# Kernel tuning notes

Measured on AMD Instinct MI355X. Metric: run time of the kernel, lower is better.

## Reference

```python
import jax, jax.numpy as jnp
import numpy as np

T, B, D, H = 2048, 64, 512, 512

def setup_inputs() -> dict:
    key = jax.random.key(0)
    ks = jax.random.split(key, 5)
    scale = 1.0 / np.sqrt(D + H)  # ~ torch Linear init scale
    inputs = jax.random.normal(ks[0], (T, B, D), dtype=jnp.float32)
    Wf = jax.random.normal(ks[1], (D + H, H), dtype=jnp.float32) * scale
    Wi = jax.random.normal(ks[2], (D + H, H), dtype=jnp.float32) * scale
    Wg = jax.random.normal(ks[3], (D + H, H), dtype=jnp.float32) * scale
    Wo = jax.random.normal(ks[4], (D + H, H), dtype=jnp.float32) * scale
    z = jnp.zeros((H,), dtype=jnp.float32)
    return {"inputs": inputs, "Wf": Wf, "bf": z, "Wi": Wi, "bi": z,
            "Wg": Wg, "bg": z, "Wo": Wo, "bo": z}

def reference(inputs, Wf, bf, Wi, bi, Wg, bg, Wo, bo):
    # Fuse the 4 gate GEMMs into one [D+H, 4H] matmul per step (same math).
    W = jnp.concatenate([Wf, Wi, Wg, Wo], axis=1)          # [D+H, 4H]
    b = jnp.concatenate([bf, bi, bg, bo], axis=0)          # [4H]
    Hdim = Wf.shape[1]
    Bsz = inputs.shape[1]
    h0 = jnp.zeros((Bsz, Hdim), dtype=inputs.dtype)
    c0 = jnp.zeros((Bsz, Hdim), dtype=inputs.dtype)

    def step(carry, x):
        hx, cx = carry
        combined = jnp.concatenate([x, hx], axis=1)        # [B, D+H]
        gates = combined @ W + b                           # [B, 4H]
        f, i, g, o = jnp.split(gates, 4, axis=1)
        f = jax.nn.sigmoid(f)
        i = jax.nn.sigmoid(i)
        g = jnp.tanh(g)
        o = jax.nn.sigmoid(o)
        cx = f * cx + i * g
        hx = o * jnp.tanh(cx)
        return (hx, cx), hx

    (hT, cT), stacked = jax.lax.scan(step, (h0, c0), inputs)
    return stacked, (hT, cT)
```

## Files before the change

### kernel.cpp

```cpp
#include <hip/hip_runtime.h>
#include <hip/hip_bf16.h>


#define T_N 2048
#define B_N 64
#define D_N 512
#define H_N 512
#define DH_N 1024
#define NBLK 64
#define NHEAT 192
#define CPB 8
#define GCPB 32
#define NTHR 256

#define STACK_ELEMS ((size_t)T_N * B_N * H_N)
#define HT_OFF STACK_ELEMS
#define CT_OFF (STACK_ELEMS + (size_t)B_N * H_N)

typedef __attribute__((ext_vector_type(4))) float f32x4;
typedef __attribute__((ext_vector_type(8))) short bf16x8;

__device__ __forceinline__ unsigned short f2bf(float f) {
  union { __hip_bfloat16 h; unsigned short u; } u;
  u.h = __float2bfloat16(f);
  return u.u;
}
__device__ __forceinline__ float bf2f(unsigned short us) {
  union { unsigned u32; float f; } x;
  x.u32 = ((unsigned)us) << 16;
  return x.f;
}

__device__ __forceinline__ float sigf(float x) { return 1.0f / (1.0f + __expf(-x)); }
__device__ __forceinline__ float tanhfast(float x) { return 1.0f - 2.0f / (__expf(2.0f * x) + 1.0f); }

__global__ void init_ws_kernel(unsigned* ws32) {
  int i = blockIdx.x * blockDim.x + threadIdx.x;
  if (i < 65536) ws32[i] = 0u;
}

__global__ void xconv_kernel(const float* __restrict__ X, unsigned short* __restrict__ Xb) {
  size_t i = ((size_t)blockIdx.x * blockDim.x + threadIdx.x) * 8;
  float4 v0 = *(const float4*)(X + i);
  float4 v1 = *(const float4*)(X + i + 4);
  bf16x8 o;
  o[0] = (short)f2bf(v0.x); o[1] = (short)f2bf(v0.y);
  o[2] = (short)f2bf(v0.z); o[3] = (short)f2bf(v0.w);
  o[4] = (short)f2bf(v1.x); o[5] = (short)f2bf(v1.y);
  o[6] = (short)f2bf(v1.z); o[7] = (short)f2bf(v1.w);
  *(bf16x8*)(Xb + i) = o;
}

__device__ __forceinline__ void load_x_tile(const unsigned short* Xb, const float* X,
                                            int t, int arow, int kg, bf16x8 (&xa)[16]) {
  if (Xb) {
    const unsigned short* xp = Xb + ((size_t)t * B_N + arow) * D_N + kg;
#pragma unroll
    for (int kk = 0; kk < 16; ++kk) xa[kk] = *(const bf16x8*)(xp + kk * 32);
  } else {
    const float* xp = X + ((size_t)t * B_N + arow) * D_N + kg;
#pragma unroll
    for (int kk = 0; kk < 16; ++kk) {
      float4 v0 = *(const float4*)(xp + kk * 32);
      float4 v1 = *(const float4*)(xp + kk * 32 + 4);
      bf16x8 a;
      a[0] = (short)f2bf(v0.x); a[1] = (short)f2bf(v0.y);
      a[2] = (short)f2bf(v0.z); a[3] = (short)f2bf(v0.w);
      a[4] = (short)f2bf(v1.x); a[5] = (short)f2bf(v1.y);
      a[6] = (short)f2bf(v1.z); a[7] = (short)f2bf(v1.w);
      xa[kk] = a;
    }
  }
}

__global__ __launch_bounds__(NTHR, 1) void lstm_kernel(
    const float* __restrict__ X, const unsigned short* __restrict__ Xb,
    const float* __restrict__ Wf, const float* __restrict__ bF,
    const float* __restrict__ Wi, const float* __restrict__ bI,
    const float* __restrict__ Wg, const float* __restrict__ bG,
    const float* __restrict__ Wo, const float* __restrict__ bO,
    unsigned short* __restrict__ ring, unsigned* __restrict__ flags,
    float* __restrict__ out) {
  __shared__ unsigned short Wl[GCPB * DH_N];

  const int tid = threadIdx.x;
  const int blk = blockIdx.x;
  const int lane = tid & 63;

  if (blk >= NBLK) {
    const unsigned long long* fp = (const unsigned long long*)flags + (size_t)lane * 2;
    float a = 1.0f + (float)tid * 1e-7f;
    const float m = 0.99993f, c = 1e-8f;
    for (long i = 0;; ++i) {
#pragma unroll
      for (int j = 0; j < 512; ++j) a = __builtin_fmaf(a, m, c);
      if ((i & 63) == 0) {
        unsigned long long q0 = __hip_atomic_load(fp, __ATOMIC_RELAXED, __HIP_MEMORY_SCOPE_AGENT);
        unsigned long long q1 = __hip_atomic_load(fp + 1, __ATOMIC_RELAXED, __HIP_MEMORY_SCOPE_AGENT);
        unsigned a0 = (unsigned)q0, a1 = (unsigned)(q0 >> 32);
        unsigned a2 = (unsigned)q1, a3 = (unsigned)(q1 >> 32);
        bool ok = (a0 >= (unsigned)T_N) && (a1 >= (unsigned)T_N) &&
                  (a2 >= (unsigned)T_N) && (a3 >= (unsigned)T_N);
        if (__all((int)ok)) break;
        if (i > (1l << 21)) break;
      }
    }
    asm volatile("" :: "v"(a));
    return;
  }

  const int c0 = blk * CPB;
  const int w = tid >> 6;
  const int l16 = lane & 15;
  const int g16 = lane >> 4;

  for (int idx = tid; idx < GCPB * DH_N; idx += NTHR) {
    int k = idx >> 5;
    int cl = idx & 31;
    const float* wsrc = (cl < 8) ? Wf : (cl < 16) ? Wi : (cl < 24) ? Wg : Wo;
    float v = wsrc[(size_t)k * H_N + c0 + (cl & 7)];
    int pos = ((k >> 5) * 1024) + ((cl >> 4) * 512) + (((k >> 3) & 3) * 128) + ((cl & 15) * 8) + (k & 7);
    Wl[pos] = f2bf(v);
  }

  const int cc = l16 & 7;
  const float bias0 = (l16 < 8) ? bF[c0 + cc] : bI[c0 + cc];
  const float bias1 = (l16 < 8) ? bG[c0 + cc] : bO[c0 + cc];
  __syncthreads();

  const int arow = 16 * w + l16;
  const int kg = 8 * g16;
  const int lofs8 = lane * 8;
  const bool owner = (arow == blk);

  bf16x8 wb0[32], wb1[32];
#pragma unroll
  for (int K = 0; K < 32; ++K) {
    wb0[K] = *(const bf16x8*)&Wl[K * 1024 + lofs8];
    wb1[K] = *(const bf16x8*)&Wl[K * 1024 + 512 + lofs8];
  }

  float cst[4] = {0.f, 0.f, 0.f, 0.f};
  float hT_local[4] = {0.f, 0.f, 0.f, 0.f};

  bf16x8 xa[16];
  load_x_tile(Xb, X, 0, arow, kg, xa);

  for (int t = 0; t < T_N; ++t) {
    const int slotR = (t + 1) & 1;
    const int slotW = t & 1;

    f32x4 x0a = {0.f,0.f,0.f,0.f}, x0b = {0.f,0.f,0.f,0.f};
    f32x4 x1a = {0.f,0.f,0.f,0.f}, x1b = {0.f,0.f,0.f,0.f};
#pragma unroll
    for (int kk = 0; kk < 8; ++kk) {
      x0a = __builtin_amdgcn_mfma_f32_16x16x32_bf16(xa[kk], wb0[kk], x0a, 0, 0, 0);
      x1a = __builtin_amdgcn_mfma_f32_16x16x32_bf16(xa[kk], wb1[kk], x1a, 0, 0, 0);
    }
#pragma unroll
    for (int kk = 8; kk < 16; ++kk) {
      x0b = __builtin_amdgcn_mfma_f32_16x16x32_bf16(xa[kk], wb0[kk], x0b, 0, 0, 0);
      x1b = __builtin_amdgcn_mfma_f32_16x16x32_bf16(xa[kk], wb1[kk], x1b, 0, 0, 0);
    }

    if (t > 0) {
      const unsigned tgt = (unsigned)t;
      const unsigned long long* fp = (const unsigned long long*)flags + (size_t)lane * 2;
      long guard = 0;
      for (;;) {
        unsigned long long q0 = __hip_atomic_load(fp, __ATOMIC_RELAXED, __HIP_MEMORY_SCOPE_AGENT);
        unsigned long long q1 = __hip_atomic_load(fp + 1, __ATOMIC_RELAXED, __HIP_MEMORY_SCOPE_AGENT);
        unsigned a0 = (unsigned)q0, a1 = (unsigned)(q0 >> 32);
        unsigned a2 = (unsigned)q1, a3 = (unsigned)(q1 >> 32);
        bool ok = (a0 >= tgt) && (a1 >= tgt) && (a2 >= tgt) && (a3 >= tgt);
        if (__all((int)ok)) break;
        __builtin_amdgcn_s_sleep(1);
        if (++guard > (1l << 22)) break;
      }
    }

    unsigned long long hq0[16], hq1[16];
    {
      const unsigned long long* hbase =
          (const unsigned long long*)(ring + (size_t)slotR * (B_N * H_N));
#pragma unroll
      for (int kk = 0; kk < 16; ++kk) {
        const unsigned long long* hp = hbase + (size_t)(g16 + 4 * kk) * 128 + arow * 2;
        hq0[kk] = __hip_atomic_load(hp, __ATOMIC_RELAXED, __HIP_MEMORY_SCOPE_AGENT);
        hq1[kk] = __hip_atomic_load(hp + 1, __ATOMIC_RELAXED, __HIP_MEMORY_SCOPE_AGENT);
      }
    }

    f32x4 h0a = {0.f,0.f,0.f,0.f}, h0b = {0.f,0.f,0.f,0.f};
    f32x4 h1a = {0.f,0.f,0.f,0.f}, h1b = {0.f,0.f,0.f,0.f};
#pragma unroll
    for (int kk = 0; kk < 8; ++kk) {
      union { unsigned long long q[2]; bf16x8 v; } u;
      u.q[0] = hq0[kk]; u.q[1] = hq1[kk];
      h0a = __builtin_amdgcn_mfma_f32_16x16x32_bf16(u.v, wb0[16 + kk], h0a, 0, 0, 0);
      h1a = __builtin_amdgcn_mfma_f32_16x16x32_bf16(u.v, wb1[16 + kk], h1a, 0, 0, 0);
    }
#pragma unroll
    for (int kk = 8; kk < 16; ++kk) {
      union { unsigned long long q[2]; bf16x8 v; } u;
      u.q[0] = hq0[kk]; u.q[1] = hq1[kk];
      h0b = __builtin_amdgcn_mfma_f32_16x16x32_bf16(u.v, wb0[16 + kk], h0b, 0, 0, 0);
      h1b = __builtin_amdgcn_mfma_f32_16x16x32_bf16(u.v, wb1[16 + kk], h1b, 0, 0, 0);
    }
    f32x4 m0v = (x0a + x0b) + (h0a + h0b);
    f32x4 m1v = (x1a + x1b) + (h1a + h1b);

    const bool lo = (l16 < 8);
    float hv[4];
#pragma unroll
    for (int r = 0; r < 4; ++r) {
      float m0 = m0v[r] + bias0;
      float m1 = m1v[r] + bias1;
      float p0 = __shfl_xor(m0, 8, 64);
      float p1 = __shfl_xor(m1, 8, 64);
      float fv = lo ? m0 : p0;
      float iv = lo ? p0 : m0;
      float gv = lo ? m1 : p1;
      float ov = lo ? p1 : m1;
      float f = sigf(fv), i = sigf(iv), g = tanhfast(gv), o = sigf(ov);
      float c = f * cst[r] + i * g;
      cst[r] = c;
      hv[r] = o * tanhfast(c);
    }

    {
      unsigned* rb = (unsigned*)(ring + (size_t)slotW * (B_N * H_N) + (size_t)blk * 512);
#pragma unroll
      for (int r = 0; r < 4; ++r) {
        int row = 16 * w + 4 * g16 + r;
        unsigned short hb = f2bf(hv[r]);
        unsigned opp = __shfl_xor((unsigned)hb, 1, 64);
        if (lo && (cc & 1) == 0) {
          unsigned pack = (unsigned)hb | (opp << 16);
          __hip_atomic_store(rb + row * 4 + (cc >> 1), pack,
                             __ATOMIC_RELAXED, __HIP_MEMORY_SCOPE_AGENT);
        }
      }
    }

    asm volatile("s_waitcnt vmcnt(0)" ::: "memory");
    if (lane == 0) {
      __hip_atomic_store(flags + blk * 4 + w, (unsigned)(t + 1),
                         __ATOMIC_RELAXED, __HIP_MEMORY_SCOPE_AGENT);
    }

    if (t + 1 < T_N) load_x_tile(Xb, X, t + 1, arow, kg, xa);

    if (owner && t > 0) {
      float* oprev = out + (size_t)(t - 1) * (B_N * H_N) + (size_t)blk * H_N + kg;
#pragma unroll
      for (int kk = 0; kk < 16; ++kk) {
        union { unsigned long long q[2]; bf16x8 v; } u;
        u.q[0] = hq0[kk]; u.q[1] = hq1[kk];
        float4 f0, f1;
        f0.x = bf2f((unsigned short)u.v[0]); f0.y = bf2f((unsigned short)u.v[1]);
        f0.z = bf2f((unsigned short)u.v[2]); f0.w = bf2f((unsigned short)u.v[3]);
        f1.x = bf2f((unsigned short)u.v[4]); f1.y = bf2f((unsigned short)u.v[5]);
        f1.z = bf2f((unsigned short)u.v[6]); f1.w = bf2f((unsigned short)u.v[7]);
        *(float4*)(oprev + kk * 32) = f0;
        *(float4*)(oprev + kk * 32 + 4) = f1;
      }
    }

    if (t == T_N - 1) {
      float* obase = out + (size_t)t * (B_N * H_N);
#pragma unroll
      for (int r = 0; r < 4; ++r) {
        int row = 16 * w + 4 * g16 + r;
        if (lo) obase[(size_t)row * H_N + c0 + cc] = hv[r];
        hT_local[r] = hv[r];
      }
    }
  }

  if (l16 < 8) {
#pragma unroll
    for (int r = 0; r < 4; ++r) {
      int row = 16 * w + 4 * g16 + r;
      out[HT_OFF + (size_t)row * H_N + c0 + cc] = hT_local[r];
      out[CT_OFF + (size_t)row * H_N + c0 + cc] = cst[r];
    }
  }
}

extern "C" void kernel_launch(void* const* d_in, const int* in_sizes, int n_in,
                              void* d_out, int out_size, void* d_ws, size_t ws_size,
                              hipStream_t stream) {
  const float* X  = (const float*)d_in[0];
  const float* Wf = (const float*)d_in[1];
  const float* bF = (const float*)d_in[2];
  const float* Wi = (const float*)d_in[3];
  const float* bI = (const float*)d_in[4];
  const float* Wg = (const float*)d_in[5];
  const float* bG = (const float*)d_in[6];
  const float* Wo = (const float*)d_in[7];
  const float* bO = (const float*)d_in[8];
  float* out = (float*)d_out;

  unsigned char* ws = (unsigned char*)d_ws;
  unsigned* flags = (unsigned*)(ws + 1024);
  unsigned short* ring = (unsigned short*)(ws + 32768);
  const size_t xb_off = 262144;
  const size_t need_xb = xb_off + (size_t)T_N * B_N * D_N * 2;
  unsigned short* Xb = (ws_size >= need_xb) ? (unsigned short*)(ws + xb_off) : nullptr;

  init_ws_kernel<<<dim3(256), dim3(256), 0, stream>>>((unsigned*)ws);
  if (Xb) {
    xconv_kernel<<<dim3((T_N * B_N * D_N) / 8 / 256), dim3(256), 0, stream>>>(X, Xb);
  }
  lstm_kernel<<<dim3(NBLK + NHEAT), dim3(NTHR), 0, stream>>>(
      X, Xb, Wf, bF, Wi, bI, Wg, bG, Wo, bO, ring, flags, out);
}
```

Before: 11.10 ms.

## Write output directly from producer blocks and signal heater exit via done counter

Each block now writes its own freshly computed h values (rounded to bf16, widened to fp32) straight to the stacked output at step t, split across lo/hi lanes. This replaces the owner-row path that re-wrote row t-1 from the gathered ring data. It also skips the recurrent MFMA and the flag wait at t=0, and heater blocks now exit on a single done counter that each compute block increments when it finishes, instead of polling all the flags. The output writes are spread more evenly across blocks, which removes one block's serial store tail, but each step now issues more scattered 8-byte global stores.

```diff
diff --git a/kernel.cpp b/kernel.cpp
--- a/kernel.cpp
+++ b/kernel.cpp
@@ -6,16 +6,21 @@
 #define B_N 64
 #define D_N 512
 #define H_N 512
-#define DH_N 1024
 #define NBLK 64
 #define NHEAT 192
 #define CPB 8
 #define GCPB 32
 #define NTHR 256
+#define BH (B_N * H_N)
 
 #define STACK_ELEMS ((size_t)T_N * B_N * H_N)
 #define HT_OFF STACK_ELEMS
 #define CT_OFF (STACK_ELEMS + (size_t)B_N * H_N)
+
+#define WS_DONE 0
+#define WS_FLAGS 1024
+#define WS_MIRROR 32768
+#define WS_XB 262144
 
 typedef __attribute__((ext_vector_type(4))) float f32x4;
 typedef __attribute__((ext_vector_type(8))) short bf16x8;
@@ -25,12 +30,6 @@
   u.h = __float2bfloat16(f);
   return u.u;
 }
-__device__ __forceinline__ float bf2f(unsigned short us) {
-  union { unsigned u32; float f; } x;
-  x.u32 = ((unsigned)us) << 16;
-  return x.f;
-}
-
 __device__ __forceinline__ float sigf(float x) { return 1.0f / (1.0f + __expf(-x)); }
 __device__ __forceinline__ float tanhfast(float x) { return 1.0f - 2.0f / (__expf(2.0f * x) + 1.0f); }
 
@@ -79,30 +78,24 @@
     const float* __restrict__ Wi, const float* __restrict__ bI,
     const float* __restrict__ Wg, const float* __restrict__ bG,
     const float* __restrict__ Wo, const float* __restrict__ bO,
-    unsigned short* __restrict__ ring, unsigned* __restrict__ flags,
-    float* __restrict__ out) {
-  __shared__ unsigned short Wl[GCPB * DH_N];
+    unsigned char* wsb, float* __restrict__ out) {
+  __shared__ unsigned short Wl[GCPB * (D_N + H_N)];
 
   const int tid = threadIdx.x;
   const int blk = blockIdx.x;
   const int lane = tid & 63;
 
   if (blk >= NBLK) {
-    const unsigned long long* fp = (const unsigned long long*)flags + (size_t)lane * 2;
-    float a = 1.0f + (float)tid * 1e-7f;
-    const float m = 0.99993f, c = 1e-8f;
+    const unsigned* dp = (const unsigned*)(wsb + WS_DONE);
+    float a = 1.0f + (float)(blk * NTHR + tid) * 1e-7f;
+    const float hm = 0.99993f, hc = 1e-8f;
     for (long i = 0;; ++i) {
 #pragma unroll
-      for (int j = 0; j < 512; ++j) a = __builtin_fmaf(a, m, c);
-      if ((i & 63) == 0) {
-        unsigned long long q0 = __hip_atomic_load(fp, __ATOMIC_RELAXED, __HIP_MEMORY_SCOPE_AGENT);
-        unsigned long long q1 = __hip_atomic_load(fp + 1, __ATOMIC_RELAXED, __HIP_MEMORY_SCOPE_AGENT);
-        unsigned a0 = (unsigned)q0, a1 = (unsigned)(q0 >> 32);
-        unsigned a2 = (unsigned)q1, a3 = (unsigned)(q1 >> 32);
-        bool ok = (a0 >= (unsigned)T_N) && (a1 >= (unsigned)T_N) &&
-                  (a2 >= (unsigned)T_N) && (a3 >= (unsigned)T_N);
-        if (__all((int)ok)) break;
-        if (i > (1l << 21)) break;
+      for (int j = 0; j < 512; ++j) a = __builtin_fmaf(a, hm, hc);
+      if ((i & 7) == 0) {
+        unsigned d = __hip_atomic_load(dp, __ATOMIC_RELAXED, __HIP_MEMORY_SCOPE_AGENT);
+        if (d >= (unsigned)NBLK) break;
+        if (i > (1l << 20)) break;
       }
     }
     asm volatile("" :: "v"(a));
@@ -113,8 +106,10 @@
   const int w = tid >> 6;
   const int l16 = lane & 15;
   const int g16 = lane >> 4;
-
-  for (int idx = tid; idx < GCPB * DH_N; idx += NTHR) {
+  const int cc = l16 & 7;
+  const bool lo = (l16 < 8);
+
+  for (int idx = tid; idx < GCPB * (D_N + H_N); idx += NTHR) {
     int k = idx >> 5;
     int cl = idx & 31;
     const float* wsrc = (cl < 8) ? Wf : (cl < 16) ? Wi : (cl < 24) ? Wg : Wo;
@@ -122,16 +117,13 @@
     int pos = ((k >> 5) * 1024) + ((cl >> 4) * 512) + (((k >> 3) & 3) * 128) + ((cl & 15) * 8) + (k & 7);
     Wl[pos] = f2bf(v);
   }
-
-  const int cc = l16 & 7;
-  const float bias0 = (l16 < 8) ? bF[c0 + cc] : bI[c0 + cc];
-  const float bias1 = (l16 < 8) ? bG[c0 + cc] : bO[c0 + cc];
+  const float bias0 = lo ? bF[c0 + cc] : bI[c0 + cc];
+  const float bias1 = lo ? bG[c0 + cc] : bO[c0 + cc];
   __syncthreads();
 
   const int arow = 16 * w + l16;
   const int kg = 8 * g16;
   const int lofs8 = lane * 8;
-  const bool owner = (arow == blk);
 
   bf16x8 wb0[32], wb1[32];
 #pragma unroll
@@ -140,6 +132,7 @@
     wb1[K] = *(const bf16x8*)&Wl[K * 1024 + 512 + lofs8];
   }
 
+  unsigned* flags = (unsigned*)(wsb + WS_FLAGS);
   float cst[4] = {0.f, 0.f, 0.f, 0.f};
   float hT_local[4] = {0.f, 0.f, 0.f, 0.f};
 
@@ -150,8 +143,7 @@
     const int slotR = (t + 1) & 1;
     const int slotW = t & 1;
 
-    f32x4 x0a = {0.f,0.f,0.f,0.f}, x0b = {0.f,0.f,0.f,0.f};
-    f32x4 x1a = {0.f,0.f,0.f,0.f}, x1b = {0.f,0.f,0.f,0.f};
+    f32x4 x0a = {0,0,0,0}, x0b = {0,0,0,0}, x1a = {0,0,0,0}, x1b = {0,0,0,0};
 #pragma unroll
     for (int kk = 0; kk < 8; ++kk) {
       x0a = __builtin_amdgcn_mfma_f32_16x16x32_bf16(xa[kk], wb0[kk], x0a, 0, 0, 0);
@@ -163,54 +155,58 @@
       x1b = __builtin_amdgcn_mfma_f32_16x16x32_bf16(xa[kk], wb1[kk], x1b, 0, 0, 0);
     }
 
+    f32x4 m0v, m1v;
     if (t > 0) {
-      const unsigned tgt = (unsigned)t;
-      const unsigned long long* fp = (const unsigned long long*)flags + (size_t)lane * 2;
-      long guard = 0;
-      for (;;) {
-        unsigned long long q0 = __hip_atomic_load(fp, __ATOMIC_RELAXED, __HIP_MEMORY_SCOPE_AGENT);
-        unsigned long long q1 = __hip_atomic_load(fp + 1, __ATOMIC_RELAXED, __HIP_MEMORY_SCOPE_AGENT);
-        unsigned a0 = (unsigned)q0, a1 = (unsigned)(q0 >> 32);
-        unsigned a2 = (unsigned)q1, a3 = (unsigned)(q1 >> 32);
-        bool ok = (a0 >= tgt) && (a1 >= tgt) && (a2 >= tgt) && (a3 >= tgt);
-        if (__all((int)ok)) break;
-        __builtin_amdgcn_s_sleep(1);
-        if (++guard > (1l << 22)) break;
-      }
-    }
-
-    unsigned long long hq0[16], hq1[16];
-    {
-      const unsigned long long* hbase =
-          (const unsigned long long*)(ring + (size_t)slotR * (B_N * H_N));
-#pragma unroll
-      for (int kk = 0; kk < 16; ++kk) {
-        const unsigned long long* hp = hbase + (size_t)(g16 + 4 * kk) * 128 + arow * 2;
-        hq0[kk] = __hip_atomic_load(hp, __ATOMIC_RELAXED, __HIP_MEMORY_SCOPE_AGENT);
-        hq1[kk] = __hip_atomic_load(hp + 1, __ATOMIC_RELAXED, __HIP_MEMORY_SCOPE_AGENT);
-      }
-    }
-
-    f32x4 h0a = {0.f,0.f,0.f,0.f}, h0b = {0.f,0.f,0.f,0.f};
-    f32x4 h1a = {0.f,0.f,0.f,0.f}, h1b = {0.f,0.f,0.f,0.f};
-#pragma unroll
-    for (int kk = 0; kk < 8; ++kk) {
-      union { unsigned long long q[2]; bf16x8 v; } u;
-      u.q[0] = hq0[kk]; u.q[1] = hq1[kk];
-      h0a = __builtin_amdgcn_mfma_f32_16x16x32_bf16(u.v, wb0[16 + kk], h0a, 0, 0, 0);
-      h1a = __builtin_amdgcn_mfma_f32_16x16x32_bf16(u.v, wb1[16 + kk], h1a, 0, 0, 0);
-    }
-#pragma unroll
-    for (int kk = 8; kk < 16; ++kk) {
-      union { unsigned long long q[2]; bf16x8 v; } u;
-      u.q[0] = hq0[kk]; u.q[1] = hq1[kk];
-      h0b = __builtin_amdgcn_mfma_f32_16x16x32_bf16(u.v, wb0[16 + kk], h0b, 0, 0, 0);
-      h1b = __builtin_amdgcn_mfma_f32_16x16x32_bf16(u.v, wb1[16 + kk], h1b, 0, 0, 0);
-    }
-    f32x4 m0v = (x0a + x0b) + (h0a + h0b);
-    f32x4 m1v = (x1a + x1b) + (h1a + h1b);
-
-    const bool lo = (l16 < 8);
+      {
+        const unsigned tgt = (unsigned)t;
+        const unsigned long long* fp = (const unsigned long long*)flags + (size_t)lane * 2;
+        long guard = 0;
+        for (;;) {
+          unsigned long long q0 = __hip_atomic_load(fp, __ATOMIC_RELAXED, __HIP_MEMORY_SCOPE_AGENT);
+          unsigned long long q1 = __hip_atomic_load(fp + 1, __ATOMIC_RELAXED, __HIP_MEMORY_SCOPE_AGENT);
+          unsigned a0 = (unsigned)q0, a1 = (unsigned)(q0 >> 32);
+          unsigned a2 = (unsigned)q1, a3 = (unsigned)(q1 >> 32);
+          bool ok = (a0 >= tgt) && (a1 >= tgt) && (a2 >= tgt) && (a3 >= tgt);
+          if (__all((int)ok)) break;
+          __builtin_amdgcn_s_sleep(1);
+          if (++guard > (1l << 22)) break;
+        }
+      }
+
+      unsigned long long hq0[16], hq1[16];
+      {
+        const unsigned long long* hbase =
+            (const unsigned long long*)(wsb + WS_MIRROR + (size_t)slotR * 65536);
+#pragma unroll
+        for (int kk = 0; kk < 16; ++kk) {
+          const unsigned long long* hp = hbase + (size_t)(g16 + 4 * kk) * 128 + arow * 2;
+          hq0[kk] = __hip_atomic_load(hp, __ATOMIC_RELAXED, __HIP_MEMORY_SCOPE_AGENT);
+          hq1[kk] = __hip_atomic_load(hp + 1, __ATOMIC_RELAXED, __HIP_MEMORY_SCOPE_AGENT);
+        }
+      }
+
+      f32x4 h0a = {0,0,0,0}, h0b = {0,0,0,0}, h1a = {0,0,0,0}, h1b = {0,0,0,0};
+#pragma unroll
+      for (int kk = 0; kk < 8; ++kk) {
+        union { unsigned long long q[2]; bf16x8 v; } u;
+        u.q[0] = hq0[kk]; u.q[1] = hq1[kk];
+        h0a = __builtin_amdgcn_mfma_f32_16x16x32_bf16(u.v, wb0[16 + kk], h0a, 0, 0, 0);
+        h1a = __builtin_amdgcn_mfma_f32_16x16x32_bf16(u.v, wb1[16 + kk], h1a, 0, 0, 0);
+      }
+#pragma unroll
+      for (int kk = 8; kk < 16; ++kk) {
+        union { unsigned long long q[2]; bf16x8 v; } u;
+        u.q[0] = hq0[kk]; u.q[1] = hq1[kk];
+        h0b = __builtin_amdgcn_mfma_f32_16x16x32_bf16(u.v, wb0[16 + kk], h0b, 0, 0, 0);
+        h1b = __builtin_amdgcn_mfma_f32_16x16x32_bf16(u.v, wb1[16 + kk], h1b, 0, 0, 0);
+      }
+      m0v = (x0a + x0b) + (h0a + h0b);
+      m1v = (x1a + x1b) + (h1a + h1b);
+    } else {
+      m0v = x0a + x0b;
+      m1v = x1a + x1b;
+    }
+
     float hv[4];
 #pragma unroll
     for (int r = 0; r < 4; ++r) {
@@ -229,16 +225,21 @@
     }
 
     {
-      unsigned* rb = (unsigned*)(ring + (size_t)slotW * (B_N * H_N) + (size_t)blk * 512);
+      unsigned* mrb = (unsigned*)(wsb + WS_MIRROR + (size_t)slotW * 65536) + blk * 256;
+      float* outt = out + (size_t)t * BH + c0;
 #pragma unroll
       for (int r = 0; r < 4; ++r) {
         int row = 16 * w + 4 * g16 + r;
         unsigned short hb = f2bf(hv[r]);
         unsigned opp = __shfl_xor((unsigned)hb, 1, 64);
-        if (lo && (cc & 1) == 0) {
+        bool mine = ((cc & 1) == 0) && (lo ? (r < 2) : (r >= 2));
+        if (mine) {
           unsigned pack = (unsigned)hb | (opp << 16);
-          __hip_atomic_store(rb + row * 4 + (cc >> 1), pack,
+          __hip_atomic_store(mrb + row * 4 + (cc >> 1), pack,
                              __ATOMIC_RELAXED, __HIP_MEMORY_SCOPE_AGENT);
+          unsigned long long ov = ((unsigned long long)((unsigned)hb << 16)) |
+                                  (((unsigned long long)(opp << 16)) << 32);
+          *(unsigned long long*)(outt + (size_t)row * H_N + cc) = ov;
         }
       }
     }
@@ -251,34 +252,13 @@
 
     if (t + 1 < T_N) load_x_tile(Xb, X, t + 1, arow, kg, xa);
 
-    if (owner && t > 0) {
-      float* oprev = out + (size_t)(t - 1) * (B_N * H_N) + (size_t)blk * H_N + kg;
-#pragma unroll
-      for (int kk = 0; kk < 16; ++kk) {
-        union { unsigned long long q[2]; bf16x8 v; } u;
-        u.q[0] = hq0[kk]; u.q[1] = hq1[kk];
-        float4 f0, f1;
-        f0.x = bf2f((unsigned short)u.v[0]); f0.y = bf2f((unsigned short)u.v[1]);
-        f0.z = bf2f((unsigned short)u.v[2]); f0.w = bf2f((unsigned short)u.v[3]);
-        f1.x = bf2f((unsigned short)u.v[4]); f1.y = bf2f((unsigned short)u.v[5]);
-        f1.z = bf2f((unsigned short)u.v[6]); f1.w = bf2f((unsigned short)u.v[7]);
-        *(float4*)(oprev + kk * 32) = f0;
-        *(float4*)(oprev + kk * 32 + 4) = f1;
-      }
-    }
-
     if (t == T_N - 1) {
-      float* obase = out + (size_t)t * (B_N * H_N);
-#pragma unroll
-      for (int r = 0; r < 4; ++r) {
-        int row = 16 * w + 4 * g16 + r;
-        if (lo) obase[(size_t)row * H_N + c0 + cc] = hv[r];
-        hT_local[r] = hv[r];
-      }
-    }
-  }
-
-  if (l16 < 8) {
+#pragma unroll
+      for (int r = 0; r < 4; ++r) hT_local[r] = hv[r];
+    }
+  }
+
+  if (lo) {
 #pragma unroll
     for (int r = 0; r < 4; ++r) {
       int row = 16 * w + 4 * g16 + r;
@@ -286,6 +266,10 @@
       out[CT_OFF + (size_t)row * H_N + c0 + cc] = cst[r];
     }
   }
+  __syncthreads();
+  if (tid == 0)
+    __hip_atomic_fetch_add((unsigned*)(wsb + WS_DONE), 1u,
+                           __ATOMIC_RELAXED, __HIP_MEMORY_SCOPE_AGENT);
 }
 
 extern "C" void kernel_launch(void* const* d_in, const int* in_sizes, int n_in,
@@ -303,16 +287,13 @@
   float* out = (float*)d_out;
 
   unsigned char* ws = (unsigned char*)d_ws;
-  unsigned* flags = (unsigned*)(ws + 1024);
-  unsigned short* ring = (unsigned short*)(ws + 32768);
-  const size_t xb_off = 262144;
-  const size_t need_xb = xb_off + (size_t)T_N * B_N * D_N * 2;
-  unsigned short* Xb = (ws_size >= need_xb) ? (unsigned short*)(ws + xb_off) : nullptr;
+  const size_t need_xb = WS_XB + (size_t)T_N * B_N * D_N * 2;
+  unsigned short* Xb = (ws_size >= need_xb) ? (unsigned short*)(ws + WS_XB) : nullptr;
 
   init_ws_kernel<<<dim3(256), dim3(256), 0, stream>>>((unsigned*)ws);
   if (Xb) {
     xconv_kernel<<<dim3((T_N * B_N * D_N) / 8 / 256), dim3(256), 0, stream>>>(X, Xb);
   }
   lstm_kernel<<<dim3(NBLK + NHEAT), dim3(NTHR), 0, stream>>>(
-      X, Xb, Wf, bF, Wi, bI, Wg, bG, Wo, bO, ring, flags, out);
-}
+      X, Xb, Wf, bF, Wi, bI, Wg, bG, Wo, bO, ws, out);
+}
```

Measured after the change: 12.21 ms. +10.0%, slower.
